# Kernel optimization log

Measured on AMD Instinct MI355X. Metric: run time of the kernel, lower is better.

Reference implementation:

```python
import jax, jax.numpy as jnp
import numpy as np


def setup_inputs() -> dict:
    key = jax.random.key(0)
    k1, k2 = jax.random.split(key)
    B, D, N = 8, 256, 64
    x = jax.random.normal(k1, (B, D, N), dtype=jnp.float32)
    W = jax.random.normal(k2, (N, 3 * N), dtype=jnp.float32) * (1.0 / np.sqrt(N))
    return {"x": x, "W": W}


def reference(x, W):
    # x: [B, D, N], W: [N, 3N] (Dense on last axis, no bias)
    B, D, N = x.shape
    qkv = jnp.einsum('bdn,nm->bdm', x, W)            # [B, D, 3N]
    q, k, v = qkv[..., :N], qkv[..., N:2 * N], qkv[..., 2 * N:]
    scale = 1.0 / jnp.sqrt(jnp.asarray(N, dtype=x.dtype))
    # per-channel rank-1 attention: scores[b,n,i,j] = q[b,i,n]*k[b,j,n]
    scores = jnp.einsum('bin,bjn->bnij', q, k) * scale  # [B, N, D, D]
    attn = jax.nn.softmax(scores, axis=-1)
    out = jnp.einsum('bnij,bjn->bin', attn, v)          # [B, D, N]
    return out
```

## Files before the change

### kernel.cpp

```cpp
#include <hip/hip_runtime.h>
#include <math.h>

#define NB 8
#define ND 256
#define NN 64

__global__ __launch_bounds__(256, 2)
void fused_mhsa_kernel(const float* __restrict__ x,
                       const float* __restrict__ W,
                       float* __restrict__ out) {
    const int bn = blockIdx.x;
    const int b  = bn >> 6;
    const int n  = bn & 63;
    const int i  = threadIdx.x;

    __shared__ float wq[NN], wk[NN], wv[NN];
    __shared__ __align__(16) float ks[ND];
    __shared__ __align__(16) float vs[ND];
    __shared__ float red[8];

    if (i < 3 * NN) {
        const int which = i >> 6;
        const int m     = i & 63;
        const float val = W[m * (3 * NN) + which * NN + n];
        if (which == 0)      wq[m] = val;
        else if (which == 1) wk[m] = val;
        else                 wv[m] = val;
    }
    __syncthreads();

    const float4* xrow = reinterpret_cast<const float4*>(x + ((size_t)b * ND + i) * NN);
    float q = 0.f, k = 0.f, v = 0.f;
    #pragma unroll
    for (int m4 = 0; m4 < NN / 4; ++m4) {
        const float4 xv = xrow[m4];
        const int m = m4 * 4;
        q = fmaf(xv.x, wq[m+0], q); k = fmaf(xv.x, wk[m+0], k); v = fmaf(xv.x, wv[m+0], v);
        q = fmaf(xv.y, wq[m+1], q); k = fmaf(xv.y, wk[m+1], k); v = fmaf(xv.y, wv[m+1], v);
        q = fmaf(xv.z, wq[m+2], q); k = fmaf(xv.z, wk[m+2], k); v = fmaf(xv.z, wv[m+2], v);
        q = fmaf(xv.w, wq[m+3], q); k = fmaf(xv.w, wk[m+3], k); v = fmaf(xv.w, wv[m+3], v);
    }
    ks[i] = k;
    vs[i] = v;

    float kmax = k, kmin = k;
    #pragma unroll
    for (int off = 32; off > 0; off >>= 1) {
        kmax = fmaxf(kmax, __shfl_xor(kmax, off));
        kmin = fminf(kmin, __shfl_xor(kmin, off));
    }
    const int wave = i >> 6;
    if ((i & 63) == 0) { red[wave] = kmax; red[4 + wave] = kmin; }
    __syncthreads();
    kmax = fmaxf(fmaxf(red[0], red[1]), fmaxf(red[2], red[3]));
    kmin = fminf(fminf(red[4], red[5]), fminf(red[6], red[7]));

    const float LOG2E = 1.4426950408889634f;
    const float scale = 0.125f;
    const float qs = q * scale * LOG2E;
    const float m2 = fmaxf(qs * kmax, qs * kmin);

    float sum = 0.f, acc = 0.f;
    const float4* k4 = reinterpret_cast<const float4*>(ks);
    const float4* v4 = reinterpret_cast<const float4*>(vs);
    #pragma unroll 4
    for (int j4 = 0; j4 < ND / 4; ++j4) {
        const float4 kv = k4[j4];
        const float4 vv = v4[j4];
        const float e0 = __builtin_amdgcn_exp2f(fmaf(qs, kv.x, -m2));
        const float e1 = __builtin_amdgcn_exp2f(fmaf(qs, kv.y, -m2));
        const float e2 = __builtin_amdgcn_exp2f(fmaf(qs, kv.z, -m2));
        const float e3 = __builtin_amdgcn_exp2f(fmaf(qs, kv.w, -m2));
        sum += (e0 + e1) + (e2 + e3);
        acc = fmaf(e0, vv.x, acc);
        acc = fmaf(e1, vv.y, acc);
        acc = fmaf(e2, vv.z, acc);
        acc = fmaf(e3, vv.w, acc);
    }

    out[((size_t)b * ND + i) * NN + n] = acc / sum;
}

extern "C" void kernel_launch(void* const* d_in, const int* in_sizes, int n_in,
                              void* d_out, int out_size, void* d_ws, size_t ws_size,
                              hipStream_t stream) {
    const float* x = (const float*)d_in[0];
    const float* W = (const float*)d_in[1];
    float* out = (float*)d_out;

    dim3 grid(NB * NN);
    dim3 block(ND);
    fused_mhsa_kernel<<<grid, block, 0, stream>>>(x, W, out);
}
```

Before: 15.51 us.

## Split softmax key loop across four thread groups per block

Launches 1024 threads per block, so four groups each process a quarter of the key/value positions for the same row. Partial sums and accumulators are combined through shared memory before the final division. This raises wave count and shortens the serial exp loop. The price is recomputing the QKV projection in every group plus an extra barrier and shared-memory reduction.

```diff
diff --git a/kernel.cpp b/kernel.cpp
--- a/kernel.cpp
+++ b/kernel.cpp
@@ -4,24 +4,30 @@
 #define NB 8
 #define ND 256
 #define NN 64
+#define GROUPS 4
+#define JT (ND / GROUPS)
 
-__global__ __launch_bounds__(256, 2)
+__global__ __launch_bounds__(1024, 8)
 void fused_mhsa_kernel(const float* __restrict__ x,
                        const float* __restrict__ W,
                        float* __restrict__ out) {
     const int bn = blockIdx.x;
     const int b  = bn >> 6;
     const int n  = bn & 63;
-    const int i  = threadIdx.x;
+    const int t  = threadIdx.x;
+    const int i  = t & 255;
+    const int g  = t >> 8;
 
     __shared__ float wq[NN], wk[NN], wv[NN];
     __shared__ __align__(16) float ks[ND];
     __shared__ __align__(16) float vs[ND];
-    __shared__ float red[8];
+    __shared__ float redmax[16], redmin[16];
+    __shared__ float psum[GROUPS][ND];
+    __shared__ float pacc[GROUPS][ND];
 
-    if (i < 3 * NN) {
-        const int which = i >> 6;
-        const int m     = i & 63;
+    if (t < 3 * NN) {
+        const int which = t >> 6;
+        const int m     = t & 63;
         const float val = W[m * (3 * NN) + which * NN + n];
         if (which == 0)      wq[m] = val;
         else if (which == 1) wk[m] = val;
@@ -31,7 +37,7 @@
 
     const float4* xrow = reinterpret_cast<const float4*>(x + ((size_t)b * ND + i) * NN);
     float q = 0.f, k = 0.f, v = 0.f;
-    #pragma unroll
+    #pragma unroll 4
     for (int m4 = 0; m4 < NN / 4; ++m4) {
         const float4 xv = xrow[m4];
         const int m = m4 * 4;
@@ -40,8 +46,7 @@
         q = fmaf(xv.z, wq[m+2], q); k = fmaf(xv.z, wk[m+2], k); v = fmaf(xv.z, wv[m+2], v);
         q = fmaf(xv.w, wq[m+3], q); k = fmaf(xv.w, wk[m+3], k); v = fmaf(xv.w, wv[m+3], v);
     }
-    ks[i] = k;
-    vs[i] = v;
+    if (g == 0) { ks[i] = k; vs[i] = v; }
 
     float kmax = k, kmin = k;
     #pragma unroll
@@ -49,36 +54,47 @@
         kmax = fmaxf(kmax, __shfl_xor(kmax, off));
         kmin = fminf(kmin, __shfl_xor(kmin, off));
     }
-    const int wave = i >> 6;
-    if ((i & 63) == 0) { red[wave] = kmax; red[4 + wave] = kmin; }
+    const int wave = t >> 6;
+    if ((t & 63) == 0) { redmax[wave] = kmax; redmin[wave] = kmin; }
     __syncthreads();
-    kmax = fmaxf(fmaxf(red[0], red[1]), fmaxf(red[2], red[3]));
-    kmin = fminf(fminf(red[4], red[5]), fminf(red[6], red[7]));
+    kmax = redmax[0]; kmin = redmin[0];
+    #pragma unroll
+    for (int w = 1; w < 16; ++w) {
+        kmax = fmaxf(kmax, redmax[w]);
+        kmin = fminf(kmin, redmin[w]);
+    }
 
     const float LOG2E = 1.4426950408889634f;
     const float scale = 0.125f;
     const float qs = q * scale * LOG2E;
-    const float m2 = fmaxf(qs * kmax, qs * kmin);
+    const float nm2 = -fmaxf(qs * kmax, qs * kmin);
 
     float sum = 0.f, acc = 0.f;
-    const float4* k4 = reinterpret_cast<const float4*>(ks);
-    const float4* v4 = reinterpret_cast<const float4*>(vs);
+    const float4* k4 = reinterpret_cast<const float4*>(ks) + g * (JT / 4);
+    const float4* v4 = reinterpret_cast<const float4*>(vs) + g * (JT / 4);
     #pragma unroll 4
-    for (int j4 = 0; j4 < ND / 4; ++j4) {
+    for (int j4 = 0; j4 < JT / 4; ++j4) {
         const float4 kv = k4[j4];
         const float4 vv = v4[j4];
-        const float e0 = __builtin_amdgcn_exp2f(fmaf(qs, kv.x, -m2));
-        const float e1 = __builtin_amdgcn_exp2f(fmaf(qs, kv.y, -m2));
-        const float e2 = __builtin_amdgcn_exp2f(fmaf(qs, kv.z, -m2));
-        const float e3 = __builtin_amdgcn_exp2f(fmaf(qs, kv.w, -m2));
+        const float e0 = __builtin_amdgcn_exp2f(fmaf(qs, kv.x, nm2));
+        const float e1 = __builtin_amdgcn_exp2f(fmaf(qs, kv.y, nm2));
+        const float e2 = __builtin_amdgcn_exp2f(fmaf(qs, kv.z, nm2));
+        const float e3 = __builtin_amdgcn_exp2f(fmaf(qs, kv.w, nm2));
         sum += (e0 + e1) + (e2 + e3);
         acc = fmaf(e0, vv.x, acc);
         acc = fmaf(e1, vv.y, acc);
         acc = fmaf(e2, vv.z, acc);
         acc = fmaf(e3, vv.w, acc);
     }
+    psum[g][i] = sum;
+    pacc[g][i] = acc;
+    __syncthreads();
 
-    out[((size_t)b * ND + i) * NN + n] = acc / sum;
+    if (t < ND) {
+        float s = psum[0][t] + psum[1][t] + psum[2][t] + psum[3][t];
+        float a = pacc[0][t] + pacc[1][t] + pacc[2][t] + pacc[3][t];
+        out[((size_t)b * ND + t) * NN + n] = a / s;
+    }
 }
 
 extern "C" void kernel_launch(void* const* d_in, const int* in_sizes, int n_in,
@@ -89,6 +105,6 @@
     float* out = (float*)d_out;
 
     dim3 grid(NB * NN);
-    dim3 block(ND);
+    dim3 block(GROUPS * ND);
     fused_mhsa_kernel<<<grid, block, 0, stream>>>(x, W, out);
 }
```

New measurement: 26.73 us. +72.4%, slower.

## Split each (batch, channel) softmax across four blocks with 16-way key partitioning

Applied to the files above, without the earlier changes.

Launches four blocks per (batch, channel) pair. Each block handles a quarter of the query rows, and each thread computes partial softmax sums for 4 rows over 16 keys; the partials are then combined with warp shuffles. W columns are now read straight from global memory instead of being staged in shared memory. The aim is a shorter serial exp loop per thread and more blocks in flight. The cost is that every block recomputes the full q/k/v projection for all 256 rows, which quadruples projection work, plus the extra shuffle reductions.

```diff
diff --git a/kernel.cpp b/kernel.cpp
--- a/kernel.cpp
+++ b/kernel.cpp
@@ -4,44 +4,50 @@
 #define NB 8
 #define ND 256
 #define NN 64
+#define IQ 4
+#define ROWS (ND/IQ)
+#define KST 20
 
-__global__ __launch_bounds__(256, 2)
+__global__ __launch_bounds__(256, 6)
 void fused_mhsa_kernel(const float* __restrict__ x,
                        const float* __restrict__ W,
                        float* __restrict__ out) {
-    const int bn = blockIdx.x;
-    const int b  = bn >> 6;
-    const int n  = bn & 63;
-    const int i  = threadIdx.x;
+    const int bid = blockIdx.x;
+    const int bn  = bid >> 2;
+    const int iq  = bid & 3;
+    const int b   = bn >> 6;
+    const int n   = bn & 63;
+    const int t   = threadIdx.x;
 
-    __shared__ float wq[NN], wk[NN], wv[NN];
-    __shared__ __align__(16) float ks[ND];
-    __shared__ __align__(16) float vs[ND];
+    __shared__ __align__(16) float qs[ND];
+    __shared__ __align__(16) float ks2[16][KST];
+    __shared__ __align__(16) float vs2[16][KST];
     __shared__ float red[8];
 
-    if (i < 3 * NN) {
-        const int which = i >> 6;
-        const int m     = i & 63;
-        const float val = W[m * (3 * NN) + which * NN + n];
-        if (which == 0)      wq[m] = val;
-        else if (which == 1) wk[m] = val;
-        else                 wv[m] = val;
-    }
-    __syncthreads();
-
-    const float4* xrow = reinterpret_cast<const float4*>(x + ((size_t)b * ND + i) * NN);
+    const float4* xrow = reinterpret_cast<const float4*>(x + ((size_t)b * ND + t) * NN);
+    const float* Wc = W + n;
     float q = 0.f, k = 0.f, v = 0.f;
     #pragma unroll
     for (int m4 = 0; m4 < NN / 4; ++m4) {
         const float4 xv = xrow[m4];
         const int m = m4 * 4;
-        q = fmaf(xv.x, wq[m+0], q); k = fmaf(xv.x, wk[m+0], k); v = fmaf(xv.x, wv[m+0], v);
-        q = fmaf(xv.y, wq[m+1], q); k = fmaf(xv.y, wk[m+1], k); v = fmaf(xv.y, wv[m+1], v);
-        q = fmaf(xv.z, wq[m+2], q); k = fmaf(xv.z, wk[m+2], k); v = fmaf(xv.z, wv[m+2], v);
-        q = fmaf(xv.w, wq[m+3], q); k = fmaf(xv.w, wk[m+3], k); v = fmaf(xv.w, wv[m+3], v);
+        q = fmaf(xv.x, Wc[(m+0)*192 +   0], q);
+        k = fmaf(xv.x, Wc[(m+0)*192 +  64], k);
+        v = fmaf(xv.x, Wc[(m+0)*192 + 128], v);
+        q = fmaf(xv.y, Wc[(m+1)*192 +   0], q);
+        k = fmaf(xv.y, Wc[(m+1)*192 +  64], k);
+        v = fmaf(xv.y, Wc[(m+1)*192 + 128], v);
+        q = fmaf(xv.z, Wc[(m+2)*192 +   0], q);
+        k = fmaf(xv.z, Wc[(m+2)*192 +  64], k);
+        v = fmaf(xv.z, Wc[(m+2)*192 + 128], v);
+        q = fmaf(xv.w, Wc[(m+3)*192 +   0], q);
+        k = fmaf(xv.w, Wc[(m+3)*192 +  64], k);
+        v = fmaf(xv.w, Wc[(m+3)*192 + 128], v);
     }
-    ks[i] = k;
-    vs[i] = v;
+    const float LOG2E = 1.4426950408889634f;
+    qs[t] = q * (0.125f * LOG2E);
+    ks2[t >> 4][t & 15] = k;
+    vs2[t >> 4][t & 15] = v;
 
     float kmax = k, kmin = k;
     #pragma unroll
@@ -49,36 +55,61 @@
         kmax = fmaxf(kmax, __shfl_xor(kmax, off));
         kmin = fminf(kmin, __shfl_xor(kmin, off));
     }
-    const int wave = i >> 6;
-    if ((i & 63) == 0) { red[wave] = kmax; red[4 + wave] = kmin; }
+    const int wave = t >> 6;
+    if ((t & 63) == 0) { red[wave] = kmax; red[4 + wave] = kmin; }
     __syncthreads();
     kmax = fmaxf(fmaxf(red[0], red[1]), fmaxf(red[2], red[3]));
     kmin = fminf(fminf(red[4], red[5]), fminf(red[6], red[7]));
 
-    const float LOG2E = 1.4426950408889634f;
-    const float scale = 0.125f;
-    const float qs = q * scale * LOG2E;
-    const float m2 = fmaxf(qs * kmax, qs * kmin);
+    const int jg = t & 15;
+    const int rs = t >> 4;
 
-    float sum = 0.f, acc = 0.f;
-    const float4* k4 = reinterpret_cast<const float4*>(ks);
-    const float4* v4 = reinterpret_cast<const float4*>(vs);
-    #pragma unroll 4
-    for (int j4 = 0; j4 < ND / 4; ++j4) {
-        const float4 kv = k4[j4];
-        const float4 vv = v4[j4];
-        const float e0 = __builtin_amdgcn_exp2f(fmaf(qs, kv.x, -m2));
-        const float e1 = __builtin_amdgcn_exp2f(fmaf(qs, kv.y, -m2));
-        const float e2 = __builtin_amdgcn_exp2f(fmaf(qs, kv.z, -m2));
-        const float e3 = __builtin_amdgcn_exp2f(fmaf(qs, kv.w, -m2));
-        sum += (e0 + e1) + (e2 + e3);
-        acc = fmaf(e0, vv.x, acc);
-        acc = fmaf(e1, vv.y, acc);
-        acc = fmaf(e2, vv.z, acc);
-        acc = fmaf(e3, vv.w, acc);
+    const float4 q4 = *reinterpret_cast<const float4*>(&qs[iq * ROWS + rs * 4]);
+    const float qm0 = q4.x, qm1 = q4.y, qm2 = q4.z, qm3 = q4.w;
+    const float nm0 = -fmaxf(qm0 * kmax, qm0 * kmin);
+    const float nm1 = -fmaxf(qm1 * kmax, qm1 * kmin);
+    const float nm2 = -fmaxf(qm2 * kmax, qm2 * kmin);
+    const float nm3 = -fmaxf(qm3 * kmax, qm3 * kmin);
+
+    float s0 = 0.f, s1 = 0.f, s2 = 0.f, s3 = 0.f;
+    float a0 = 0.f, a1 = 0.f, a2 = 0.f, a3 = 0.f;
+    #pragma unroll
+    for (int c = 0; c < 4; ++c) {
+        const float4 kc = *reinterpret_cast<const float4*>(&ks2[jg][c * 4]);
+        const float4 vc = *reinterpret_cast<const float4*>(&vs2[jg][c * 4]);
+        float e;
+        e = __builtin_amdgcn_exp2f(fmaf(qm0, kc.x, nm0)); s0 += e; a0 = fmaf(e, vc.x, a0);
+        e = __builtin_amdgcn_exp2f(fmaf(qm0, kc.y, nm0)); s0 += e; a0 = fmaf(e, vc.y, a0);
+        e = __builtin_amdgcn_exp2f(fmaf(qm0, kc.z, nm0)); s0 += e; a0 = fmaf(e, vc.z, a0);
+        e = __builtin_amdgcn_exp2f(fmaf(qm0, kc.w, nm0)); s0 += e; a0 = fmaf(e, vc.w, a0);
+        e = __builtin_amdgcn_exp2f(fmaf(qm1, kc.x, nm1)); s1 += e; a1 = fmaf(e, vc.x, a1);
+        e = __builtin_amdgcn_exp2f(fmaf(qm1, kc.y, nm1)); s1 += e; a1 = fmaf(e, vc.y, a1);
+        e = __builtin_amdgcn_exp2f(fmaf(qm1, kc.z, nm1)); s1 += e; a1 = fmaf(e, vc.z, a1);
+        e = __builtin_amdgcn_exp2f(fmaf(qm1, kc.w, nm1)); s1 += e; a1 = fmaf(e, vc.w, a1);
+        e = __builtin_amdgcn_exp2f(fmaf(qm2, kc.x, nm2)); s2 += e; a2 = fmaf(e, vc.x, a2);
+        e = __builtin_amdgcn_exp2f(fmaf(qm2, kc.y, nm2)); s2 += e; a2 = fmaf(e, vc.y, a2);
+        e = __builtin_amdgcn_exp2f(fmaf(qm2, kc.z, nm2)); s2 += e; a2 = fmaf(e, vc.z, a2);
+        e = __builtin_amdgcn_exp2f(fmaf(qm2, kc.w, nm2)); s2 += e; a2 = fmaf(e, vc.w, a2);
+        e = __builtin_amdgcn_exp2f(fmaf(qm3, kc.x, nm3)); s3 += e; a3 = fmaf(e, vc.x, a3);
+        e = __builtin_amdgcn_exp2f(fmaf(qm3, kc.y, nm3)); s3 += e; a3 = fmaf(e, vc.y, a3);
+        e = __builtin_amdgcn_exp2f(fmaf(qm3, kc.z, nm3)); s3 += e; a3 = fmaf(e, vc.z, a3);
+        e = __builtin_amdgcn_exp2f(fmaf(qm3, kc.w, nm3)); s3 += e; a3 = fmaf(e, vc.w, a3);
     }
 
-    out[((size_t)b * ND + i) * NN + n] = acc / sum;
+    #pragma unroll
+    for (int off = 1; off < 16; off <<= 1) {
+        s0 += __shfl_xor(s0, off); a0 += __shfl_xor(a0, off);
+        s1 += __shfl_xor(s1, off); a1 += __shfl_xor(a1, off);
+        s2 += __shfl_xor(s2, off); a2 += __shfl_xor(a2, off);
+        s3 += __shfl_xor(s3, off); a3 += __shfl_xor(a3, off);
+    }
+
+    if (jg < 4) {
+        const float av = (jg == 0) ? a0 : (jg == 1) ? a1 : (jg == 2) ? a2 : a3;
+        const float sv = (jg == 0) ? s0 : (jg == 1) ? s1 : (jg == 2) ? s2 : s3;
+        const int row = iq * ROWS + rs * 4 + jg;
+        out[((size_t)b * ND + row) * NN + n] = av / sv;
+    }
 }
 
 extern "C" void kernel_launch(void* const* d_in, const int* in_sizes, int n_in,
@@ -88,7 +119,7 @@
     const float* W = (const float*)d_in[1];
     float* out = (float*)d_out;
 
-    dim3 grid(NB * NN);
+    dim3 grid(NB * NN * IQ);
     dim3 block(ND);
     fused_mhsa_kernel<<<grid, block, 0, stream>>>(x, W, out);
 }
```

Measured after the change: 24.04 us. +55.0%, slower.

## Split softmax key range across two thread halves per block

Applied to the files above, without the earlier changes.

Doubles the block to 512 threads so each query row's 256-key softmax loop is split into two halves of 128 keys, computed by separate threads. Partial sums and accumulators are combined through shared memory after an extra barrier. The q projection is stored to shared memory so both halves can read it, and the inner loop keeps two independent accumulator chains to add ILP. The projection phase now leaves half the threads idle, and the split adds one synchronization.

```diff
diff --git a/kernel.cpp b/kernel.cpp
--- a/kernel.cpp
+++ b/kernel.cpp
@@ -4,24 +4,30 @@
 #define NB 8
 #define ND 256
 #define NN 64
+#define NT 512
+#define JH 128
 
-__global__ __launch_bounds__(256, 2)
+__global__ __launch_bounds__(NT, 4)
 void fused_mhsa_kernel(const float* __restrict__ x,
                        const float* __restrict__ W,
                        float* __restrict__ out) {
     const int bn = blockIdx.x;
     const int b  = bn >> 6;
     const int n  = bn & 63;
-    const int i  = threadIdx.x;
+    const int t  = threadIdx.x;
+    const int i  = t & 255;
+    const int h  = t >> 8;
 
     __shared__ float wq[NN], wk[NN], wv[NN];
+    __shared__ __align__(16) float qs[ND];
     __shared__ __align__(16) float ks[ND];
     __shared__ __align__(16) float vs[ND];
     __shared__ float red[8];
+    __shared__ float psum1[ND], pacc1[ND];
 
-    if (i < 3 * NN) {
-        const int which = i >> 6;
-        const int m     = i & 63;
+    if (t < 3 * NN) {
+        const int which = t >> 6;
+        const int m     = t & 63;
         const float val = W[m * (3 * NN) + which * NN + n];
         if (which == 0)      wq[m] = val;
         else if (which == 1) wk[m] = val;
@@ -29,19 +35,23 @@
     }
     __syncthreads();
 
-    const float4* xrow = reinterpret_cast<const float4*>(x + ((size_t)b * ND + i) * NN);
-    float q = 0.f, k = 0.f, v = 0.f;
-    #pragma unroll
-    for (int m4 = 0; m4 < NN / 4; ++m4) {
-        const float4 xv = xrow[m4];
-        const int m = m4 * 4;
-        q = fmaf(xv.x, wq[m+0], q); k = fmaf(xv.x, wk[m+0], k); v = fmaf(xv.x, wv[m+0], v);
-        q = fmaf(xv.y, wq[m+1], q); k = fmaf(xv.y, wk[m+1], k); v = fmaf(xv.y, wv[m+1], v);
-        q = fmaf(xv.z, wq[m+2], q); k = fmaf(xv.z, wk[m+2], k); v = fmaf(xv.z, wv[m+2], v);
-        q = fmaf(xv.w, wq[m+3], q); k = fmaf(xv.w, wk[m+3], k); v = fmaf(xv.w, wv[m+3], v);
+    float k = 0.f;
+    if (t < ND) {
+        const float4* xrow = reinterpret_cast<const float4*>(x + ((size_t)b * ND + t) * NN);
+        float q = 0.f, v = 0.f;
+        #pragma unroll
+        for (int m4 = 0; m4 < NN / 4; ++m4) {
+            const float4 xv = xrow[m4];
+            const int m = m4 * 4;
+            q = fmaf(xv.x, wq[m+0], q); k = fmaf(xv.x, wk[m+0], k); v = fmaf(xv.x, wv[m+0], v);
+            q = fmaf(xv.y, wq[m+1], q); k = fmaf(xv.y, wk[m+1], k); v = fmaf(xv.y, wv[m+1], v);
+            q = fmaf(xv.z, wq[m+2], q); k = fmaf(xv.z, wk[m+2], k); v = fmaf(xv.z, wv[m+2], v);
+            q = fmaf(xv.w, wq[m+3], q); k = fmaf(xv.w, wk[m+3], k); v = fmaf(xv.w, wv[m+3], v);
+        }
+        qs[t] = q * (0.125f * 1.4426950408889634f);
+        ks[t] = k;
+        vs[t] = v;
     }
-    ks[i] = k;
-    vs[i] = v;
 
     float kmax = k, kmin = k;
     #pragma unroll
@@ -49,36 +59,43 @@
         kmax = fmaxf(kmax, __shfl_xor(kmax, off));
         kmin = fminf(kmin, __shfl_xor(kmin, off));
     }
-    const int wave = i >> 6;
-    if ((i & 63) == 0) { red[wave] = kmax; red[4 + wave] = kmin; }
+    if (t < ND && (t & 63) == 0) { red[t >> 6] = kmax; red[4 + (t >> 6)] = kmin; }
     __syncthreads();
     kmax = fmaxf(fmaxf(red[0], red[1]), fmaxf(red[2], red[3]));
     kmin = fminf(fminf(red[4], red[5]), fminf(red[6], red[7]));
 
-    const float LOG2E = 1.4426950408889634f;
-    const float scale = 0.125f;
-    const float qs = q * scale * LOG2E;
-    const float m2 = fmaxf(qs * kmax, qs * kmin);
+    const float qv = qs[i];
+    const float nm = -fmaxf(qv * kmax, qv * kmin);
 
-    float sum = 0.f, acc = 0.f;
-    const float4* k4 = reinterpret_cast<const float4*>(ks);
-    const float4* v4 = reinterpret_cast<const float4*>(vs);
-    #pragma unroll 4
-    for (int j4 = 0; j4 < ND / 4; ++j4) {
-        const float4 kv = k4[j4];
-        const float4 vv = v4[j4];
-        const float e0 = __builtin_amdgcn_exp2f(fmaf(qs, kv.x, -m2));
-        const float e1 = __builtin_amdgcn_exp2f(fmaf(qs, kv.y, -m2));
-        const float e2 = __builtin_amdgcn_exp2f(fmaf(qs, kv.z, -m2));
-        const float e3 = __builtin_amdgcn_exp2f(fmaf(qs, kv.w, -m2));
-        sum += (e0 + e1) + (e2 + e3);
-        acc = fmaf(e0, vv.x, acc);
-        acc = fmaf(e1, vv.y, acc);
-        acc = fmaf(e2, vv.z, acc);
-        acc = fmaf(e3, vv.w, acc);
+    const float4* k4 = reinterpret_cast<const float4*>(ks) + h * (JH / 4);
+    const float4* v4 = reinterpret_cast<const float4*>(vs) + h * (JH / 4);
+
+    float sA = 0.f, sB = 0.f, aA = 0.f, aB = 0.f;
+    #pragma unroll
+    for (int jj = 0; jj < JH / 8; ++jj) {
+        const float4 ka = k4[jj * 2 + 0];
+        const float4 kb = k4[jj * 2 + 1];
+        const float4 va = v4[jj * 2 + 0];
+        const float4 vb = v4[jj * 2 + 1];
+        float e;
+        e = __builtin_amdgcn_exp2f(fmaf(qv, ka.x, nm)); sA += e; aA = fmaf(e, va.x, aA);
+        e = __builtin_amdgcn_exp2f(fmaf(qv, ka.y, nm)); sA += e; aA = fmaf(e, va.y, aA);
+        e = __builtin_amdgcn_exp2f(fmaf(qv, ka.z, nm)); sA += e; aA = fmaf(e, va.z, aA);
+        e = __builtin_amdgcn_exp2f(fmaf(qv, ka.w, nm)); sA += e; aA = fmaf(e, va.w, aA);
+        e = __builtin_amdgcn_exp2f(fmaf(qv, kb.x, nm)); sB += e; aB = fmaf(e, vb.x, aB);
+        e = __builtin_amdgcn_exp2f(fmaf(qv, kb.y, nm)); sB += e; aB = fmaf(e, vb.y, aB);
+        e = __builtin_amdgcn_exp2f(fmaf(qv, kb.z, nm)); sB += e; aB = fmaf(e, vb.z, aB);
+        e = __builtin_amdgcn_exp2f(fmaf(qv, kb.w, nm)); sB += e; aB = fmaf(e, vb.w, aB);
     }
+    const float s = sA + sB;
+    const float a = aA + aB;
 
-    out[((size_t)b * ND + i) * NN + n] = acc / sum;
+    if (h == 1) { psum1[i] = s; pacc1[i] = a; }
+    __syncthreads();
+
+    if (t < ND) {
+        out[((size_t)b * ND + t) * NN + n] = (a + pacc1[t]) / (s + psum1[t]);
+    }
 }
 
 extern "C" void kernel_launch(void* const* d_in, const int* in_sizes, int n_in,
@@ -89,6 +106,6 @@
     float* out = (float*)d_out;
 
     dim3 grid(NB * NN);
-    dim3 block(ND);
+    dim3 block(NT);
     fused_mhsa_kernel<<<grid, block, 0, stream>>>(x, W, out);
 }
```

New measurement: 15.18 us. 2.1% less time.
